# Performance work log

Hardware: AMD Instinct MI355X
Metric: run time of the kernel (lower is better)

The kernel has to match this reference:

```python
import jax, jax.numpy as jnp
import numpy as np

B, T, N, M, D = 4, 64, 16, 8, 512

def setup_inputs() -> dict:
    key = jax.random.key(0)
    ks = jax.random.split(key, 7)
    s = 1.0 / np.sqrt(D)
    return {
        "x": jax.random.normal(ks[0], (B, T, N, M, D), dtype=jnp.float32),
        "Wq": jax.random.normal(ks[1], (D, D), dtype=jnp.float32) * s,
        "bq": jax.random.normal(ks[2], (D,), dtype=jnp.float32) * s,
        "Wk": jax.random.normal(ks[3], (D, D), dtype=jnp.float32) * s,
        "bk": jax.random.normal(ks[4], (D,), dtype=jnp.float32) * s,
        "Wv": jax.random.normal(ks[5], (D, D), dtype=jnp.float32) * s,
        "bv": jax.random.normal(ks[6], (D,), dtype=jnp.float32) * s,
    }

def reference(x, Wq, bq, Wk, bk, Wv, bv):
    # Linear projections (torch Linear: y = x @ W^T + b)
    Q = jnp.einsum('btnmd,ed->btnme', x, Wq) + bq
    K = jnp.einsum('btnmd,ed->btnme', x, Wk) + bk
    V = jnp.einsum('btnmd,ed->btnme', x, Wv) + bv
    scale = 1.0 / jnp.sqrt(jnp.asarray(Q.shape[-1], Q.dtype))
    # contract over batch b AND feature d -> shared attention over modality axis m
    attn_score = jnp.einsum('btnmd,btnkd->tnmk', Q, K) * scale  # [t,n,m,m]
    attn_weight = jax.nn.softmax(attn_score, axis=-1)
    return jnp.einsum('tnmk,btnkd->btnmd', attn_weight, V)
```

## Files before the change

### kernel.cpp

```cpp
#include <hip/hip_runtime.h>

#define Bb 4
#define Tt 64
#define Nn 16
#define Mm 8
#define Dd 512
#define RR 32
#define QSTR 520

typedef __attribute__((ext_vector_type(8))) short bf16x8;
typedef __attribute__((ext_vector_type(16))) float f32x16;

__device__ __forceinline__ unsigned short f2bf(float f) {
    union { float f; unsigned int u; } v; v.f = f;
    unsigned int r = (v.u + 0x7fffu + ((v.u >> 16) & 1u)) >> 16;
    return (unsigned short)r;
}
__device__ __forceinline__ float bf2f(unsigned short h) {
    union { unsigned int u; float f; } v; v.u = ((unsigned int)h) << 16;
    return v.f;
}

__global__ __launch_bounds__(256) void convert_w_kernel(
    const float* __restrict__ Wq, const float* __restrict__ Wk,
    const float* __restrict__ Wv, unsigned short* __restrict__ Wb)
{
    int idx = blockIdx.x * 256 + threadIdx.x;
    int flat = idx << 2;
    int row = flat >> 9;
    int d = flat & 511;
    const float* src = (row < 512) ? Wq : ((row < 1024) ? Wk : Wv);
    int r = row & 511;
    float4 v = *(const float4*)(src + r * Dd + d);
    ushort4 o;
    o.x = f2bf(v.x); o.y = f2bf(v.y); o.z = f2bf(v.z); o.w = f2bf(v.w);
    int e = row >> 5, n = row & 31;
    int kk = d >> 4, hi = (d >> 3) & 1, j = d & 7;
    *(ushort4*)(Wb + ((((e * 32 + kk) * 64) + hi * 32 + n) << 3) + j) = o;
}

__global__ __launch_bounds__(1024, 4) void fused_attn_kernel(
    const float* __restrict__ x, const unsigned short* __restrict__ Wb,
    const float* __restrict__ bq, const float* __restrict__ bk,
    const float* __restrict__ bv, float* __restrict__ out)
{
    __shared__ unsigned short lds_x[RR * QSTR];
    __shared__ unsigned short lds_qkv[3 * RR * QSTR];
    __shared__ float lds_p[Mm * Mm];

    const int tid = threadIdx.x;
    const int t = blockIdx.x >> 4;
    const int n = blockIdx.x & 15;

    #pragma unroll
    for (int i = 0; i < 4; ++i) {
        int fi = i * 1024 + tid;
        int flat = fi << 2;
        int row = flat >> 9;
        int d = flat & 511;
        int b = row >> 3, m = row & 7;
        float4 v = *(const float4*)(x + ((((long)(b * Tt + t)) * Nn + n) * Mm + m) * Dd + d);
        ushort4 o;
        o.x = f2bf(v.x); o.y = f2bf(v.y); o.z = f2bf(v.z); o.w = f2bf(v.w);
        *(ushort4*)(&lds_x[row * QSTR + d]) = o;
    }
    __syncthreads();

    const int lane = tid & 63;
    const int wave = tid >> 6;
    const int arow = lane & 31;
    const int ahalf = lane >> 5;

    {
        const int e0 = wave * 3;
        const unsigned short* wp0 = Wb + (long)e0 * 16384 + lane * 8;
        const unsigned short* wp1 = wp0 + 16384;
        const unsigned short* wp2 = wp1 + 16384;

        bf16x8 pb[2][3];
        #pragma unroll
        for (int i = 0; i < 2; ++i) {
            pb[i][0] = *(const bf16x8*)(wp0 + i * 512);
            pb[i][1] = *(const bf16x8*)(wp1 + i * 512);
            pb[i][2] = *(const bf16x8*)(wp2 + i * 512);
        }

        f32x16 acc0 = {0.f}, acc1 = {0.f}, acc2 = {0.f};
        #pragma unroll
        for (int r = 0; r < 16; ++r) { acc0[r] = 0.f; acc1[r] = 0.f; acc2[r] = 0.f; }

        const unsigned short* abase = &lds_x[arow * QSTR + ahalf * 8];

        #pragma unroll
        for (int kk = 0; kk < 32; ++kk) {
            int cur = kk & 1;
            bf16x8 b0 = pb[cur][0];
            bf16x8 b1 = pb[cur][1];
            bf16x8 b2 = pb[cur][2];
            if (kk < 30) {
                pb[cur][0] = *(const bf16x8*)(wp0 + (kk + 2) * 512);
                pb[cur][1] = *(const bf16x8*)(wp1 + (kk + 2) * 512);
                pb[cur][2] = *(const bf16x8*)(wp2 + (kk + 2) * 512);
            }
            bf16x8 a = *(const bf16x8*)(abase + kk * 16);
            acc0 = __builtin_amdgcn_mfma_f32_32x32x16_bf16(a, b0, acc0, 0, 0, 0);
            acc1 = __builtin_amdgcn_mfma_f32_32x32x16_bf16(a, b1, acc1, 0, 0, 0);
            acc2 = __builtin_amdgcn_mfma_f32_32x32x16_bf16(a, b2, acc2, 0, 0, 0);
        }

        #pragma unroll
        for (int s = 0; s < 3; ++s) {
            f32x16 acc = (s == 0) ? acc0 : ((s == 1) ? acc1 : acc2);
            int ecol = (e0 + s) * 32 + arow;
            int proj = ecol >> 9;
            int f = ecol & 511;
            const float* bp = (proj == 0) ? bq : ((proj == 1) ? bk : bv);
            float bias = bp[f];
            unsigned short* qbase = &lds_qkv[(proj * RR) * QSTR + f];
            #pragma unroll
            for (int r = 0; r < 16; ++r) {
                int mrow = (r & 3) + 8 * (r >> 2) + 4 * ahalf;
                qbase[mrow * QSTR] = f2bf(acc[r] + bias);
            }
        }
    }
    __syncthreads();

    {
        int p = tid >> 4;
        int j = tid & 15;
        int sm = p >> 3;
        int sk = p & 7;
        float part = 0.f;
        #pragma unroll
        for (int b4 = 0; b4 < 4; ++b4) {
            const unsigned short* qr = &lds_qkv[(0 * RR + b4 * 8 + sm) * QSTR];
            const unsigned short* kr = &lds_qkv[(1 * RR + b4 * 8 + sk) * QSTR];
            #pragma unroll
            for (int i = 0; i < 8; ++i) {
                int off = (j + i * 16) * 4;
                ushort4 qa = *(const ushort4*)(qr + off);
                ushort4 ka = *(const ushort4*)(kr + off);
                part += bf2f(qa.x) * bf2f(ka.x) + bf2f(qa.y) * bf2f(ka.y)
                      + bf2f(qa.z) * bf2f(ka.z) + bf2f(qa.w) * bf2f(ka.w);
            }
        }
        part += __shfl_xor(part, 1);
        part += __shfl_xor(part, 2);
        part += __shfl_xor(part, 4);
        part += __shfl_xor(part, 8);
        if (j == 0) lds_p[p] = part * 0.04419417382415922f;
    }
    __syncthreads();

    if (tid < 64) {
        int p = tid;
        float s = lds_p[p];
        float mx = s;
        mx = fmaxf(mx, __shfl_xor(mx, 1));
        mx = fmaxf(mx, __shfl_xor(mx, 2));
        mx = fmaxf(mx, __shfl_xor(mx, 4));
        float e = __expf(s - mx);
        float sum = e;
        sum += __shfl_xor(sum, 1);
        sum += __shfl_xor(sum, 2);
        sum += __shfl_xor(sum, 4);
        lds_p[p] = e / sum;
    }
    __syncthreads();

    {
        int d4 = tid & 127;
        int b = (tid >> 7) & 3;
        int mh = tid >> 9;
        float4 vv[8];
        #pragma unroll
        for (int k = 0; k < 8; ++k) {
            ushort4 v = *(const ushort4*)(&lds_qkv[(2 * RR + b * 8 + k) * QSTR + d4 * 4]);
            vv[k].x = bf2f(v.x); vv[k].y = bf2f(v.y);
            vv[k].z = bf2f(v.z); vv[k].w = bf2f(v.w);
        }
        #pragma unroll
        for (int mi = 0; mi < 4; ++mi) {
            int m = mh * 4 + mi;
            float4 o = {0.f, 0.f, 0.f, 0.f};
            #pragma unroll
            for (int k = 0; k < 8; ++k) {
                float w = lds_p[m * Mm + k];
                o.x += w * vv[k].x;
                o.y += w * vv[k].y;
                o.z += w * vv[k].z;
                o.w += w * vv[k].w;
            }
            *(float4*)(out + ((((long)(b * Tt + t)) * Nn + n) * Mm + m) * Dd + d4 * 4) = o;
        }
    }
}

extern "C" void kernel_launch(void* const* d_in, const int* in_sizes, int n_in,
                              void* d_out, int out_size, void* d_ws, size_t ws_size,
                              hipStream_t stream) {
    const float* x  = (const float*)d_in[0];
    const float* Wq = (const float*)d_in[1];
    const float* bq = (const float*)d_in[2];
    const float* Wk = (const float*)d_in[3];
    const float* bk = (const float*)d_in[4];
    const float* Wv = (const float*)d_in[5];
    const float* bv = (const float*)d_in[6];
    float* out = (float*)d_out;
    unsigned short* Wb = (unsigned short*)d_ws;

    convert_w_kernel<<<768, 256, 0, stream>>>(Wq, Wk, Wv, Wb);
    fused_attn_kernel<<<Tt * Nn, 1024, 0, stream>>>(x, Wb, bq, bk, bv, out);
}
```

Before: 196.9 us.

## Reassociate attention to apply softmax weights to x before V projection, two groups per block

Each block now processes two (t,n) groups and reuses each weight fragment across both. Scores are computed directly from the Q/K MFMA accumulators using lane shuffles and LDS atomics, so Q/K are never staged in LDS. Because the softmax weights are linear in V, they are applied to x first and the V projection runs afterwards straight into the output, which drops the QKV LDS buffer. The weight-convert kernel now writes output-contiguous to coalesce stores. This rounds the mixed x to bf16 once more and halves the grid, which may reduce parallelism.

```diff
diff --git a/kernel.cpp b/kernel.cpp
--- a/kernel.cpp
+++ b/kernel.cpp
@@ -26,17 +26,21 @@
     const float* __restrict__ Wv, unsigned short* __restrict__ Wb)
 {
     int idx = blockIdx.x * 256 + threadIdx.x;
-    int flat = idx << 2;
-    int row = flat >> 9;
-    int d = flat & 511;
+    int o = idx << 2;
+    int j  = o & 7;
+    int n  = (o >> 3) & 31;
+    int hi = (o >> 8) & 1;
+    int ekk = o >> 9;
+    int kk = ekk & 31;
+    int e  = ekk >> 5;
+    int row = e * 32 + n;
+    int d = kk * 16 + hi * 8 + j;
     const float* src = (row < 512) ? Wq : ((row < 1024) ? Wk : Wv);
     int r = row & 511;
     float4 v = *(const float4*)(src + r * Dd + d);
-    ushort4 o;
-    o.x = f2bf(v.x); o.y = f2bf(v.y); o.z = f2bf(v.z); o.w = f2bf(v.w);
-    int e = row >> 5, n = row & 31;
-    int kk = d >> 4, hi = (d >> 3) & 1, j = d & 7;
-    *(ushort4*)(Wb + ((((e * 32 + kk) * 64) + hi * 32 + n) << 3) + j) = o;
+    ushort4 o4;
+    o4.x = f2bf(v.x); o4.y = f2bf(v.y); o4.z = f2bf(v.z); o4.w = f2bf(v.w);
+    *(ushort4*)(Wb + o) = o4;
 }
 
 __global__ __launch_bounds__(1024, 4) void fused_attn_kernel(
@@ -44,118 +48,128 @@
     const float* __restrict__ bq, const float* __restrict__ bk,
     const float* __restrict__ bv, float* __restrict__ out)
 {
-    __shared__ unsigned short lds_x[RR * QSTR];
-    __shared__ unsigned short lds_qkv[3 * RR * QSTR];
-    __shared__ float lds_p[Mm * Mm];
+    __shared__ unsigned short lds_x[2][RR * QSTR];
+    __shared__ float lds_s[2][64];
 
     const int tid = threadIdx.x;
-    const int t = blockIdx.x >> 4;
-    const int n = blockIdx.x & 15;
-
-    #pragma unroll
-    for (int i = 0; i < 4; ++i) {
-        int fi = i * 1024 + tid;
-        int flat = fi << 2;
-        int row = flat >> 9;
-        int d = flat & 511;
-        int b = row >> 3, m = row & 7;
-        float4 v = *(const float4*)(x + ((((long)(b * Tt + t)) * Nn + n) * Mm + m) * Dd + d);
-        ushort4 o;
-        o.x = f2bf(v.x); o.y = f2bf(v.y); o.z = f2bf(v.z); o.w = f2bf(v.w);
-        *(ushort4*)(&lds_x[row * QSTR + d]) = o;
-    }
-    __syncthreads();
-
     const int lane = tid & 63;
     const int wave = tid >> 6;
     const int arow = lane & 31;
     const int ahalf = lane >> 5;
 
+    const int gi0 = blockIdx.x << 1;
+    const int t = gi0 >> 4;
+    const int n0 = gi0 & 15;
+
+    const unsigned short* wq = Wb + ((long)wave << 14) + (lane << 3);
+    const unsigned short* wk = wq + (16L << 14);
+    bf16x8 pq[2], pk[2];
+    pq[0] = *(const bf16x8*)(wq);
+    pk[0] = *(const bf16x8*)(wk);
+    pq[1] = *(const bf16x8*)(wq + 512);
+    pk[1] = *(const bf16x8*)(wk + 512);
+
+    if (tid < 128) lds_s[tid >> 6][tid & 63] = 0.f;
+
+    #pragma unroll
+    for (int i = 0; i < 8; ++i) {
+        int fi = i * 1024 + tid;
+        int g = fi >> 12;
+        int rem = fi & 4095;
+        int row = rem >> 7;
+        int d = (rem & 127) << 2;
+        int b = row >> 3, m = row & 7;
+        float4 v = *(const float4*)(x + ((((long)(b * Tt + t)) * Nn + (n0 + g)) * Mm + m) * Dd + d);
+        ushort4 o;
+        o.x = f2bf(v.x); o.y = f2bf(v.y); o.z = f2bf(v.z); o.w = f2bf(v.w);
+        *(ushort4*)(&lds_x[g][row * QSTR + d]) = o;
+    }
+    __syncthreads();
+
+    const unsigned short* abase0 = &lds_x[0][arow * QSTR + (ahalf << 3)];
+    const unsigned short* abase1 = &lds_x[1][arow * QSTR + (ahalf << 3)];
+
+    f32x16 aQ0, aQ1, aK0, aK1;
+    #pragma unroll
+    for (int r = 0; r < 16; ++r) { aQ0[r] = 0.f; aQ1[r] = 0.f; aK0[r] = 0.f; aK1[r] = 0.f; }
+
+    #pragma unroll
+    for (int kk = 0; kk < 32; ++kk) {
+        int cur = kk & 1;
+        bf16x8 wqf = pq[cur];
+        bf16x8 wkf = pk[cur];
+        if (kk < 30) {
+            pq[cur] = *(const bf16x8*)(wq + (kk + 2) * 512);
+            pk[cur] = *(const bf16x8*)(wk + (kk + 2) * 512);
+        }
+        bf16x8 a0 = *(const bf16x8*)(abase0 + kk * 16);
+        bf16x8 a1 = *(const bf16x8*)(abase1 + kk * 16);
+        aQ0 = __builtin_amdgcn_mfma_f32_32x32x16_bf16(a0, wqf, aQ0, 0, 0, 0);
+        aK0 = __builtin_amdgcn_mfma_f32_32x32x16_bf16(a0, wkf, aK0, 0, 0, 0);
+        aQ1 = __builtin_amdgcn_mfma_f32_32x32x16_bf16(a1, wqf, aQ1, 0, 0, 0);
+        aK1 = __builtin_amdgcn_mfma_f32_32x32x16_bf16(a1, wkf, aK1, 0, 0, 0);
+    }
     {
-        const int e0 = wave * 3;
-        const unsigned short* wp0 = Wb + (long)e0 * 16384 + lane * 8;
-        const unsigned short* wp1 = wp0 + 16384;
-        const unsigned short* wp2 = wp1 + 16384;
-
-        bf16x8 pb[2][3];
-        #pragma unroll
-        for (int i = 0; i < 2; ++i) {
-            pb[i][0] = *(const bf16x8*)(wp0 + i * 512);
-            pb[i][1] = *(const bf16x8*)(wp1 + i * 512);
-            pb[i][2] = *(const bf16x8*)(wp2 + i * 512);
-        }
-
-        f32x16 acc0 = {0.f}, acc1 = {0.f}, acc2 = {0.f};
-        #pragma unroll
-        for (int r = 0; r < 16; ++r) { acc0[r] = 0.f; acc1[r] = 0.f; acc2[r] = 0.f; }
-
-        const unsigned short* abase = &lds_x[arow * QSTR + ahalf * 8];
-
-        #pragma unroll
-        for (int kk = 0; kk < 32; ++kk) {
-            int cur = kk & 1;
-            bf16x8 b0 = pb[cur][0];
-            bf16x8 b1 = pb[cur][1];
-            bf16x8 b2 = pb[cur][2];
-            if (kk < 30) {
-                pb[cur][0] = *(const bf16x8*)(wp0 + (kk + 2) * 512);
-                pb[cur][1] = *(const bf16x8*)(wp1 + (kk + 2) * 512);
-                pb[cur][2] = *(const bf16x8*)(wp2 + (kk + 2) * 512);
+        int f = (wave << 5) + arow;
+        float bqv = bq[f], bkv = bk[f];
+        #pragma unroll
+        for (int r = 0; r < 16; ++r) {
+            aQ0[r] += bqv; aQ1[r] += bqv;
+            aK0[r] += bkv; aK1[r] += bkv;
+        }
+    }
+
+    auto scores = [&](const f32x16& aQ, const f32x16& aK, int g) {
+        float ksw[16];
+        #pragma unroll
+        for (int r = 0; r < 16; ++r) ksw[r] = __shfl_xor(aK[r], 32);
+        #pragma unroll
+        for (int j = 0; j < 4; ++j) {
+            float v0 = 0.f, v1 = 0.f, v2 = 0.f, v3 = 0.f;
+            float v4 = 0.f, v5 = 0.f, v6 = 0.f, v7 = 0.f;
+            #pragma unroll
+            for (int b = 0; b < 4; ++b) {
+                float qv = aQ[b * 4 + j];
+                v0 += qv * aK[b * 4 + 0];  v1 += qv * aK[b * 4 + 1];
+                v2 += qv * aK[b * 4 + 2];  v3 += qv * aK[b * 4 + 3];
+                v4 += qv * ksw[b * 4 + 0]; v5 += qv * ksw[b * 4 + 1];
+                v6 += qv * ksw[b * 4 + 2]; v7 += qv * ksw[b * 4 + 3];
             }
-            bf16x8 a = *(const bf16x8*)(abase + kk * 16);
-            acc0 = __builtin_amdgcn_mfma_f32_32x32x16_bf16(a, b0, acc0, 0, 0, 0);
-            acc1 = __builtin_amdgcn_mfma_f32_32x32x16_bf16(a, b1, acc1, 0, 0, 0);
-            acc2 = __builtin_amdgcn_mfma_f32_32x32x16_bf16(a, b2, acc2, 0, 0, 0);
-        }
-
-        #pragma unroll
-        for (int s = 0; s < 3; ++s) {
-            f32x16 acc = (s == 0) ? acc0 : ((s == 1) ? acc1 : acc2);
-            int ecol = (e0 + s) * 32 + arow;
-            int proj = ecol >> 9;
-            int f = ecol & 511;
-            const float* bp = (proj == 0) ? bq : ((proj == 1) ? bk : bv);
-            float bias = bp[f];
-            unsigned short* qbase = &lds_qkv[(proj * RR) * QSTR + f];
-            #pragma unroll
-            for (int r = 0; r < 16; ++r) {
-                int mrow = (r & 3) + 8 * (r >> 2) + 4 * ahalf;
-                qbase[mrow * QSTR] = f2bf(acc[r] + bias);
+            const bool s0 = (lane & 1) != 0;
+            const bool s1 = (lane & 2) != 0;
+            const bool s2 = (lane & 4) != 0;
+            float n0v = (s0 ? v4 : v0) + __shfl_xor(s0 ? v0 : v4, 1);
+            float n1v = (s0 ? v5 : v1) + __shfl_xor(s0 ? v1 : v5, 1);
+            float n2v = (s0 ? v6 : v2) + __shfl_xor(s0 ? v2 : v6, 1);
+            float n3v = (s0 ? v7 : v3) + __shfl_xor(s0 ? v3 : v7, 1);
+            float m0v = (s1 ? n2v : n0v) + __shfl_xor(s1 ? n0v : n2v, 2);
+            float m1v = (s1 ? n3v : n1v) + __shfl_xor(s1 ? n1v : n3v, 2);
+            float u   = (s2 ? m1v : m0v) + __shfl_xor(s2 ? m0v : m1v, 4);
+            u += __shfl_xor(u, 8);
+            u += __shfl_xor(u, 16);
+            int l5 = lane & 31;
+            if (l5 < 8) {
+                int slot = (l5 & 1) * 4 + (l5 & 2) + ((l5 >> 2) & 1);
+                int m = 4 * ahalf + j;
+                int k = (slot < 4) ? (4 * ahalf + slot) : (4 * (1 - ahalf) + (slot - 4));
+                atomicAdd(&lds_s[g][m * 8 + k], u);
             }
         }
-    }
-    __syncthreads();
-
-    {
-        int p = tid >> 4;
-        int j = tid & 15;
-        int sm = p >> 3;
-        int sk = p & 7;
-        float part = 0.f;
-        #pragma unroll
-        for (int b4 = 0; b4 < 4; ++b4) {
-            const unsigned short* qr = &lds_qkv[(0 * RR + b4 * 8 + sm) * QSTR];
-            const unsigned short* kr = &lds_qkv[(1 * RR + b4 * 8 + sk) * QSTR];
-            #pragma unroll
-            for (int i = 0; i < 8; ++i) {
-                int off = (j + i * 16) * 4;
-                ushort4 qa = *(const ushort4*)(qr + off);
-                ushort4 ka = *(const ushort4*)(kr + off);
-                part += bf2f(qa.x) * bf2f(ka.x) + bf2f(qa.y) * bf2f(ka.y)
-                      + bf2f(qa.z) * bf2f(ka.z) + bf2f(qa.w) * bf2f(ka.w);
-            }
-        }
-        part += __shfl_xor(part, 1);
-        part += __shfl_xor(part, 2);
-        part += __shfl_xor(part, 4);
-        part += __shfl_xor(part, 8);
-        if (j == 0) lds_p[p] = part * 0.04419417382415922f;
-    }
-    __syncthreads();
-
-    if (tid < 64) {
-        int p = tid;
-        float s = lds_p[p];
+    };
+    scores(aQ0, aK0, 0);
+    scores(aQ1, aK1, 1);
+
+    const unsigned short* wv = Wb + ((32L + wave) << 14) + (lane << 3);
+    bf16x8 pv[4];
+    #pragma unroll
+    for (int i = 0; i < 4; ++i) pv[i] = *(const bf16x8*)(wv + i * 512);
+
+    __syncthreads();
+
+    if (tid < 128) {
+        int g = tid >> 6;
+        int p = tid & 63;
+        float s = lds_s[g][p] * 0.04419417382415922f;
         float mx = s;
         mx = fmaxf(mx, __shfl_xor(mx, 1));
         mx = fmaxf(mx, __shfl_xor(mx, 2));
@@ -165,34 +179,65 @@
         sum += __shfl_xor(sum, 1);
         sum += __shfl_xor(sum, 2);
         sum += __shfl_xor(sum, 4);
-        lds_p[p] = e / sum;
+        lds_s[g][p] = e / sum;
     }
     __syncthreads();
 
     {
         int d4 = tid & 127;
         int b = (tid >> 7) & 3;
-        int mh = tid >> 9;
-        float4 vv[8];
+        int g = tid >> 9;
+        unsigned short* xr = &lds_x[g][(b << 3) * QSTR + (d4 << 2)];
+        float4 xv[8];
         #pragma unroll
         for (int k = 0; k < 8; ++k) {
-            ushort4 v = *(const ushort4*)(&lds_qkv[(2 * RR + b * 8 + k) * QSTR + d4 * 4]);
-            vv[k].x = bf2f(v.x); vv[k].y = bf2f(v.y);
-            vv[k].z = bf2f(v.z); vv[k].w = bf2f(v.w);
-        }
-        #pragma unroll
-        for (int mi = 0; mi < 4; ++mi) {
-            int m = mh * 4 + mi;
+            ushort4 u = *(const ushort4*)(xr + k * QSTR);
+            xv[k].x = bf2f(u.x); xv[k].y = bf2f(u.y);
+            xv[k].z = bf2f(u.z); xv[k].w = bf2f(u.w);
+        }
+        ushort4 yr[8];
+        #pragma unroll
+        for (int m = 0; m < 8; ++m) {
             float4 o = {0.f, 0.f, 0.f, 0.f};
             #pragma unroll
             for (int k = 0; k < 8; ++k) {
-                float w = lds_p[m * Mm + k];
-                o.x += w * vv[k].x;
-                o.y += w * vv[k].y;
-                o.z += w * vv[k].z;
-                o.w += w * vv[k].w;
+                float w = lds_s[g][(m << 3) + k];
+                o.x += w * xv[k].x; o.y += w * xv[k].y;
+                o.z += w * xv[k].z; o.w += w * xv[k].w;
             }
-            *(float4*)(out + ((((long)(b * Tt + t)) * Nn + n) * Mm + m) * Dd + d4 * 4) = o;
+            ushort4 oy;
+            oy.x = f2bf(o.x); oy.y = f2bf(o.y); oy.z = f2bf(o.z); oy.w = f2bf(o.w);
+            yr[m] = oy;
+        }
+        #pragma unroll
+        for (int m = 0; m < 8; ++m) *(ushort4*)(xr + m * QSTR) = yr[m];
+    }
+    __syncthreads();
+
+    {
+        f32x16 aV0, aV1;
+        #pragma unroll
+        for (int r = 0; r < 16; ++r) { aV0[r] = 0.f; aV1[r] = 0.f; }
+        #pragma unroll
+        for (int kk = 0; kk < 32; ++kk) {
+            int cur = kk & 3;
+            bf16x8 wvf = pv[cur];
+            if (kk < 28) pv[cur] = *(const bf16x8*)(wv + (kk + 4) * 512);
+            bf16x8 a0 = *(const bf16x8*)(abase0 + kk * 16);
+            bf16x8 a1 = *(const bf16x8*)(abase1 + kk * 16);
+            aV0 = __builtin_amdgcn_mfma_f32_32x32x16_bf16(a0, wvf, aV0, 0, 0, 0);
+            aV1 = __builtin_amdgcn_mfma_f32_32x32x16_bf16(a1, wvf, aV1, 0, 0, 0);
+        }
+        int f = (wave << 5) + arow;
+        float bvv = bv[f];
+        float* o0 = out + f;
+        #pragma unroll
+        for (int r = 0; r < 16; ++r) {
+            int mrow = (r & 3) + 8 * (r >> 2) + 4 * ahalf;
+            int b = mrow >> 3, m = mrow & 7;
+            long base = ((((long)(b * Tt + t)) * Nn + n0) * Mm + m) * Dd;
+            o0[base] = aV0[r] + bvv;
+            o0[base + (long)Mm * Dd] = aV1[r] + bvv;
         }
     }
 }
@@ -211,5 +256,5 @@
     unsigned short* Wb = (unsigned short*)d_ws;
 
     convert_w_kernel<<<768, 256, 0, stream>>>(Wq, Wk, Wv, Wb);
-    fused_attn_kernel<<<Tt * Nn, 1024, 0, stream>>>(x, Wb, bq, bk, bv, out);
-}
+    fused_attn_kernel<<<Tt * Nn / 2, 1024, 0, stream>>>(x, Wb, bq, bk, bv, out);
+}
```

Measured after the change: 194.6 us. Within noise of the previous version (-1.2%).
